# Performance work log

Measured on AMD Instinct MI355X. Metric: run time of the kernel, lower is better.

## Reference

```python
import jax, jax.numpy as jnp
import numpy as np

B, C, T, I, R = 32, 4, 512, 64, 1024
LEAK = 0.5          # reak_rate
DENSITY = 0.1       # reservoir_density
SPECTRAL_RADIUS = 0.95
W_SCALE = 1.0       # reservoir_weights_scale
IN_SCALE = 0.1      # input_weights_scale


def setup_inputs() -> dict:
    rng = np.random.default_rng(0)
    # reservoir weights: uniform, sparsified by density mask, rescaled so the
    # largest singular value equals the target spectral radius (as in __init__)
    W = rng.uniform(-W_SCALE, W_SCALE, (R, R)).astype(np.float32)
    mask = (rng.uniform(0.0, 1.0, (R, R)) < DENSITY).astype(np.float32)
    W = W * mask
    s_max = np.linalg.svd(W, compute_uv=False).max()
    W = W * (SPECTRAL_RADIUS / s_max)
    # input weights: [R, I*C]
    Wi = rng.uniform(-IN_SCALE, IN_SCALE, (R, I * C)).astype(np.float32)

    key = jax.random.key(0)
    x = jax.random.normal(key, (B, C, T, I), dtype=jnp.float32)
    return {
        "x": x,
        "input_weights": jnp.asarray(Wi),
        "reservoir_weights": jnp.asarray(W),
    }


def reference(x, input_weights, reservoir_weights):
    # x: [B, C, T, I]
    B_, C_, T_, I_ = x.shape
    R_ = reservoir_weights.shape[0]
    # precompute the input projection for all steps: u_t = flatten(x[:,:,t,:]) @ Wi.T
    xt = jnp.transpose(x, (2, 0, 1, 3)).reshape(T_, B_, C_ * I_)  # [T, B, C*I]
    U = xt @ input_weights.T                                       # [T, B, R]

    h0 = jnp.zeros((B_, C_, R_), dtype=x.dtype)  # per-channel reservoir state

    def step(h, u):
        # leaky-integrated reservoir update; input broadcasts over channels
        h_new = LEAK * jnp.tanh(u[:, None, :] + h @ reservoir_weights) + (1.0 - LEAK) * h
        return h_new, h_new

    _, hs = jax.lax.scan(step, h0, U)            # hs: [T, B, C, R]
    return jnp.transpose(hs, (1, 2, 0, 3))       # [B, C, T, R]
```

## Files before the change

### kernel.cpp

```cpp
#include <hip/hip_runtime.h>
#include <hip/hip_bf16.h>
#include <cstdint>
#include <cstddef>


typedef unsigned short u16;
typedef unsigned int   u32;
typedef unsigned long long u64;
typedef __bf16 bf16x8 __attribute__((ext_vector_type(8)));
typedef u64    u64x2  __attribute__((ext_vector_type(2)));
typedef float  f32x4  __attribute__((ext_vector_type(4)));
typedef float  f32x2  __attribute__((ext_vector_type(2)));

#define T_STEPS 512
#define NWG     256
#define TPB     256

#define OFF_WHI 0
#define OFF_U   (2*1024*1024)
#define OFF_HB  (OFF_U + (size_t)512*32*1024*4)
#define HB_BYTES ((size_t)128*2048)
#define OFF_BAR (OFF_HB + 2*HB_BYTES)

__device__ __forceinline__ u16 f2bf(float f) {
  u32 u = __builtin_bit_cast(u32, f);
  u += 0x7fffu + ((u >> 16) & 1u);
  return (u16)(u >> 16);
}
__device__ __forceinline__ float bf2f(u16 h) {
  u32 u = ((u32)h) << 16;
  return __builtin_bit_cast(float, u);
}
__device__ __forceinline__ void pinv(bf16x8& v) { asm volatile("" : "+v"(v)); }

__device__ __forceinline__ u32 AADD(u32* p, u32 v) {
  return __hip_atomic_fetch_add(p, v, __ATOMIC_RELAXED, __HIP_MEMORY_SCOPE_AGENT);
}
__device__ __forceinline__ u32 ALD(const u32* p) {
  return __hip_atomic_load(p, __ATOMIC_RELAXED, __HIP_MEMORY_SCOPE_AGENT);
}
__device__ __forceinline__ u64 ALD64(const u64* p) {
  return __hip_atomic_load(p, __ATOMIC_RELAXED, __HIP_MEMORY_SCOPE_AGENT);
}
__device__ __forceinline__ void AST(u32* p, u32 v) {
  __hip_atomic_store(p, v, __ATOMIC_RELAXED, __HIP_MEMORY_SCOPE_AGENT);
}

__global__ void prep_w(const float* __restrict__ W, u16* __restrict__ whi) {
  int n = blockIdx.y;
  int k = blockIdx.x * 256 + threadIdx.x;
  whi[n * 1024 + k] = f2bf(W[k * 1024 + n]);
}

__global__ void __launch_bounds__(256) prep_u2(const float* __restrict__ x,
                                               const float* __restrict__ Wi,
                                               float* __restrict__ U) {
  __shared__ __align__(16) u16 Ah[128 * 128];
  __shared__ __align__(16) u16 Al[128 * 128];
  const int tid = threadIdx.x;
  const int m0 = blockIdx.x << 7;
  const int n0 = blockIdx.y << 7;
  const int wv = tid >> 6, lane = tid & 63;
  const int fc = lane & 15, kb = lane >> 4;

  f32x4 acc[8][2];
#pragma unroll
  for (int mt = 0; mt < 8; ++mt) {
    acc[mt][0] = (f32x4){0.f, 0.f, 0.f, 0.f};
    acc[mt][1] = (f32x4){0.f, 0.f, 0.f, 0.f};
  }

  for (int hf = 0; hf < 2; ++hf) {
    __syncthreads();
#pragma unroll
    for (int s = 0; s < 16; ++s) {
      int f = (s << 8) + tid;
      int row = f >> 5, v = f & 31;
      int cl = v >> 4, i4 = (v & 15) << 2;
      int b = row & 31, t = (m0 + row) >> 5;
      float4 xv = *(const float4*)(x +
          ((size_t)((b << 2) | ((hf << 1) | cl)) * 512 + t) * 64 + i4);
      int byte = (row << 8) + (((cl << 7) + (i4 << 1)) ^ ((row & 7) << 4));
      u16* ph = (u16*)((char*)Ah + byte);
      u16* pl = (u16*)((char*)Al + byte);
      float vv[4] = {xv.x, xv.y, xv.z, xv.w};
#pragma unroll
      for (int e = 0; e < 4; ++e) {
        u16 hh = f2bf(vv[e]);
        ph[e] = hh;
        pl[e] = f2bf(vv[e] - bf2f(hh));
      }
    }
    bf16x8 Bh[2][4], Bl[2][4];
#pragma unroll
    for (int nt = 0; nt < 2; ++nt) {
      const float* wrow = Wi + (size_t)(n0 + (wv << 5) + (nt << 4) + fc) * 256;
#pragma unroll
      for (int kt = 0; kt < 4; ++kt) {
        int k = (hf << 7) + (kt << 5) + (kb << 3);
        float tmp[8];
        *(float4*)&tmp[0] = *(const float4*)(wrow + k);
        *(float4*)&tmp[4] = *(const float4*)(wrow + k + 4);
#pragma unroll
        for (int e = 0; e < 8; ++e) {
          u16 hh = f2bf(tmp[e]);
          Bh[nt][kt][e] = __builtin_bit_cast(__bf16, hh);
          Bl[nt][kt][e] = __builtin_bit_cast(__bf16, f2bf(tmp[e] - bf2f(hh)));
        }
      }
    }
    __syncthreads();
#pragma unroll
    for (int kt = 0; kt < 4; ++kt) {
      int kbyte = (kt << 6) + (kb << 4);
#pragma unroll
      for (int mt = 0; mt < 8; ++mt) {
        int row = (mt << 4) + fc;
        int byte = (row << 8) + (kbyte ^ ((row & 7) << 4));
        bf16x8 ah = *(const bf16x8*)((char*)Ah + byte);
        bf16x8 al = *(const bf16x8*)((char*)Al + byte);
#pragma unroll
        for (int nt = 0; nt < 2; ++nt) {
          acc[mt][nt] = __builtin_amdgcn_mfma_f32_16x16x32_bf16(ah, Bh[nt][kt], acc[mt][nt], 0, 0, 0);
          acc[mt][nt] = __builtin_amdgcn_mfma_f32_16x16x32_bf16(al, Bh[nt][kt], acc[mt][nt], 0, 0, 0);
          acc[mt][nt] = __builtin_amdgcn_mfma_f32_16x16x32_bf16(ah, Bl[nt][kt], acc[mt][nt], 0, 0, 0);
        }
      }
    }
  }
#pragma unroll
  for (int mt = 0; mt < 8; ++mt) {
    int mbase = m0 + (mt << 4) + (kb << 2);
    int n = n0 + (wv << 5) + fc;
#pragma unroll
    for (int nt = 0; nt < 2; ++nt)
#pragma unroll
      for (int r = 0; r < 4; ++r)
        U[(size_t)(mbase + r) * 1024 + n + (nt << 4)] = acc[mt][nt][r];
  }
}

__global__ void __launch_bounds__(TPB, 1) esn_scan(
    const u16* __restrict__ Whi, const float* __restrict__ U,
    u16* __restrict__ Hb, float* __restrict__ out, u32* __restrict__ bar) {
  __shared__ __align__(16) float red[8 * 64 * 4];
  __shared__ int sh_q, sh_j, sh_loc;

  const int tid = threadIdx.x;
  const int wv = tid >> 6, lane = tid & 63;
  const int mcol = lane & 15, kb = lane >> 4;

  if (tid == 0) {
    int xcd;
    asm volatile("s_getreg_b32 %0, hwreg(HW_REG_XCC_ID)" : "=s"(xcd));
    xcd &= 7;
    AADD(bar + xcd * 64, 1u);
    AADD(bar + 512, 1u);
    while (ALD(bar + 512) < (u32)NWG) __builtin_amdgcn_s_sleep(2);
    bool uni = true;
    for (int k = 0; k < 8; ++k) uni &= (ALD(bar + k * 64) == 32u);
    if (uni) {
      sh_q = xcd;
      sh_j = (int)AADD(bar + (9 + xcd) * 64, 1u);
      sh_loc = 1;
    } else {
      sh_q = blockIdx.x & 7;
      sh_j = blockIdx.x >> 3;
      sh_loc = 0;
    }
  }
  __syncthreads();
  const int q = sh_q, j = sh_j;
  const bool xlocal = (sh_loc != 0);
  const int r0 = q << 4, c0 = j << 5;

  bf16x8 bh[2][8];
#pragma unroll
  for (int nt = 0; nt < 2; ++nt) {
    const char* wb = (const char*)Whi + (size_t)(c0 + nt * 16 + mcol) * 2048
                     + wv * 512 + kb * 16;
#pragma unroll
    for (int kt = 0; kt < 8; ++kt)
      bh[nt][kt] = *(const bf16x8*)(wb + kt * 64);
  }
#pragma unroll
  for (int nt = 0; nt < 2; ++nt)
#pragma unroll
    for (int kt = 0; kt < 8; ++kt) pinv(bh[nt][kt]);

  const int row_l = tid >> 4;
  const int col0  = (tid & 15) * 2;
  const int grow  = r0 + row_l;
  const int ont   = col0 >> 4, oci = col0 & 15;
  const int okb   = row_l >> 2, orr = row_l & 3;
  u32* flags = bar + 2048 + q * 64;

  float hreg[2] = {0.f, 0.f};
  float po0 = 0.f, po1 = 0.f;
  f32x2 uf = *(const f32x2*)(U + (size_t)(grow >> 2) * 1024 + c0 + col0);

  for (int t = 0; t < T_STEPS; ++t) {
    const char* hsrc = (const char*)Hb + (size_t)(t & 1) * HB_BYTES
                       + (size_t)(r0 + mcol) * 2048 + wv * 512 + kb * 16;
    bf16x8 av[8];
    if (xlocal) {
#pragma unroll
      for (int kt = 0; kt < 8; ++kt)
        av[kt] = *(const bf16x8*)(hsrc + kt * 64);
    } else {
#pragma unroll
      for (int kt = 0; kt < 8; ++kt) {
        u64x2 p;
        p.x = ALD64((const u64*)(hsrc + kt * 64));
        p.y = ALD64((const u64*)(hsrc + kt * 64 + 8));
        av[kt] = __builtin_bit_cast(bf16x8, p);
      }
    }
    f32x2 ufn = uf;
    if (t < T_STEPS - 1)
      ufn = *(const f32x2*)(U + ((size_t)(t + 1) * 32 + (grow >> 2)) * 1024 + c0 + col0);
    __builtin_amdgcn_sched_barrier(0);
    if (t > 0) {
      f32x2 o2; o2.x = po0; o2.y = po1;
      __builtin_nontemporal_store(o2,
          (f32x2*)(out + ((size_t)grow * 512 + (t - 1)) * 1024 + c0 + col0));
    }
    __builtin_amdgcn_sched_barrier(0);

    f32x4 acc0 = {0.f, 0.f, 0.f, 0.f};
    f32x4 acc1 = {0.f, 0.f, 0.f, 0.f};
#pragma unroll
    for (int kt = 0; kt < 8; ++kt) {
      acc0 = __builtin_amdgcn_mfma_f32_16x16x32_bf16(av[kt], bh[0][kt], acc0, 0, 0, 0);
      acc1 = __builtin_amdgcn_mfma_f32_16x16x32_bf16(av[kt], bh[1][kt], acc1, 0, 0, 0);
    }

    *(f32x4*)&red[((wv * 2 + 0) * 64 + lane) * 4] = acc0;
    *(f32x4*)&red[((wv * 2 + 1) * 64 + lane) * 4] = acc1;
    __syncthreads();

    float z0 = 0.f, z1 = 0.f;
#pragma unroll
    for (int w = 0; w < 4; ++w) {
      z0 += red[((w * 2 + ont) * 64 + okb * 16 + oci + 0) * 4 + orr];
      z1 += red[((w * 2 + ont) * 64 + okb * 16 + oci + 1) * 4 + orr];
    }
    float hn0 = 0.5f * tanhf(z0 + uf.x) + 0.5f * hreg[0];
    float hn1 = 0.5f * tanhf(z1 + uf.y) + 0.5f * hreg[1];
    hreg[0] = hn0; hreg[1] = hn1;
    po0 = hn0; po1 = hn1;

    {
      u32 pk = (u32)f2bf(hn0) | ((u32)f2bf(hn1) << 16);
      u32* hdst = (u32*)((char*)Hb + (size_t)((t + 1) & 1) * HB_BYTES
                         + (size_t)grow * 2048 + (c0 + col0) * 2);
      if (xlocal) {
        *hdst = pk;
      } else {
        (void)__hip_atomic_exchange(hdst, pk, __ATOMIC_RELAXED,
                                    __HIP_MEMORY_SCOPE_AGENT);
      }
    }
    asm volatile("s_waitcnt vmcnt(0)" ::: "memory");
    __syncthreads();

    if (t < T_STEPS - 1) {
      if (tid == 0) {
        if (xlocal) *(volatile u32*)(flags + j) = (u32)(t + 1);
        else        AST(flags + j, (u32)(t + 1));
      }
      if (wv == 0) {
        u32 tgt = (u32)(t + 1);
        if (xlocal) {
          const u32* fp = flags + (lane & 31);
          while (true) {
            u32 v = ALD(fp);
            if (__all((int)(v >= tgt))) break;
          }
          asm volatile("buffer_inv\n\ts_waitcnt vmcnt(0)" ::: "memory");
        } else {
          while (true) {
            u32 v = ALD(flags + (lane & 31));
            if (__all((int)(v >= tgt))) break;
            __builtin_amdgcn_s_sleep(1);
          }
        }
      }
      __syncthreads();
    }
    uf = ufn;
  }
  {
    f32x2 o2; o2.x = po0; o2.y = po1;
    __builtin_nontemporal_store(o2,
        (f32x2*)(out + ((size_t)grow * 512 + (T_STEPS - 1)) * 1024 + c0 + col0));
  }
}

extern "C" void kernel_launch(void* const* d_in, const int* in_sizes, int n_in,
                              void* d_out, int out_size, void* d_ws, size_t ws_size,
                              hipStream_t stream) {
  (void)in_sizes; (void)n_in; (void)out_size; (void)ws_size;
  const float* x  = (const float*)d_in[0];
  const float* Wi = (const float*)d_in[1];
  const float* W  = (const float*)d_in[2];
  float* out = (float*)d_out;

  char* ws  = (char*)d_ws;
  u16*  whi = (u16*)(ws + OFF_WHI);
  float* U  = (float*)(ws + OFF_U);
  u16*  hb  = (u16*)(ws + OFF_HB);
  u32*  bar = (u32*)(ws + OFF_BAR);

  (void)hipMemsetAsync(ws + OFF_HB, 0, 2 * HB_BYTES + 16384, stream);

  hipLaunchKernelGGL(prep_w, dim3(4, 1024), dim3(256), 0, stream, W, whi);
  hipLaunchKernelGGL(prep_u2, dim3(128, 8), dim3(256), 0, stream, x, Wi, U);
  hipLaunchKernelGGL(esn_scan, dim3(NWG), dim3(TPB), 0, stream,
                     whi, U, hb, out, bar);
}
```

Baseline: 1.435 ms.

## Replace per-block barrier with per-wave flags and double-buffered reduction scratch

Each wave now publishes its own progress flag and polls the flags of the matching waves in the other workgroups. This removes the two block-wide __syncthreads around the cross-workgroup flag exchange. The LDS reduction buffer is double-buffered by timestep parity so that dropping the trailing barrier does not cause a write-after-read hazard. H loads always use the atomic 64-bit path and the buffer_inv on the local path is removed. This risks visibility or ordering issues and adds more polling traffic, since four times as many flags are now written and polled.

```diff
diff --git a/kernel.cpp b/kernel.cpp
--- a/kernel.cpp
+++ b/kernel.cpp
@@ -143,7 +143,7 @@
 __global__ void __launch_bounds__(TPB, 1) esn_scan(
     const u16* __restrict__ Whi, const float* __restrict__ U,
     u16* __restrict__ Hb, float* __restrict__ out, u32* __restrict__ bar) {
-  __shared__ __align__(16) float red[8 * 64 * 4];
+  __shared__ __align__(16) float red[2][8 * 64 * 4];
   __shared__ int sh_q, sh_j, sh_loc;
 
   const int tid = threadIdx.x;
@@ -193,7 +193,9 @@
   const int grow  = r0 + row_l;
   const int ont   = col0 >> 4, oci = col0 & 15;
   const int okb   = row_l >> 2, orr = row_l & 3;
-  u32* flags = bar + 2048 + q * 64;
+  u32* gflags = bar + 2048 + q * 128;
+  u32* myslot = gflags + (j << 2) + wv;
+  const u32* pollp = gflags + (wv << 5) + (lane & 31);
 
   float hreg[2] = {0.f, 0.f};
   float po0 = 0.f, po1 = 0.f;
@@ -203,18 +205,12 @@
     const char* hsrc = (const char*)Hb + (size_t)(t & 1) * HB_BYTES
                        + (size_t)(r0 + mcol) * 2048 + wv * 512 + kb * 16;
     bf16x8 av[8];
-    if (xlocal) {
-#pragma unroll
-      for (int kt = 0; kt < 8; ++kt)
-        av[kt] = *(const bf16x8*)(hsrc + kt * 64);
-    } else {
-#pragma unroll
-      for (int kt = 0; kt < 8; ++kt) {
-        u64x2 p;
-        p.x = ALD64((const u64*)(hsrc + kt * 64));
-        p.y = ALD64((const u64*)(hsrc + kt * 64 + 8));
-        av[kt] = __builtin_bit_cast(bf16x8, p);
-      }
+#pragma unroll
+    for (int kt = 0; kt < 8; ++kt) {
+      u64x2 p;
+      p.x = ALD64((const u64*)(hsrc + kt * 64));
+      p.y = ALD64((const u64*)(hsrc + kt * 64 + 8));
+      av[kt] = __builtin_bit_cast(bf16x8, p);
     }
     f32x2 ufn = uf;
     if (t < T_STEPS - 1)
@@ -235,15 +231,16 @@
       acc1 = __builtin_amdgcn_mfma_f32_16x16x32_bf16(av[kt], bh[1][kt], acc1, 0, 0, 0);
     }
 
-    *(f32x4*)&red[((wv * 2 + 0) * 64 + lane) * 4] = acc0;
-    *(f32x4*)&red[((wv * 2 + 1) * 64 + lane) * 4] = acc1;
+    float* rb = red[t & 1];
+    *(f32x4*)&rb[((wv * 2 + 0) * 64 + lane) * 4] = acc0;
+    *(f32x4*)&rb[((wv * 2 + 1) * 64 + lane) * 4] = acc1;
     __syncthreads();
 
     float z0 = 0.f, z1 = 0.f;
 #pragma unroll
     for (int w = 0; w < 4; ++w) {
-      z0 += red[((w * 2 + ont) * 64 + okb * 16 + oci + 0) * 4 + orr];
-      z1 += red[((w * 2 + ont) * 64 + okb * 16 + oci + 1) * 4 + orr];
+      z0 += rb[((w * 2 + ont) * 64 + okb * 16 + oci + 0) * 4 + orr];
+      z1 += rb[((w * 2 + ont) * 64 + okb * 16 + oci + 1) * 4 + orr];
     }
     float hn0 = 0.5f * tanhf(z0 + uf.x) + 0.5f * hreg[0];
     float hn1 = 0.5f * tanhf(z1 + uf.y) + 0.5f * hreg[1];
@@ -262,31 +259,25 @@
       }
     }
     asm volatile("s_waitcnt vmcnt(0)" ::: "memory");
-    __syncthreads();
 
     if (t < T_STEPS - 1) {
-      if (tid == 0) {
-        if (xlocal) *(volatile u32*)(flags + j) = (u32)(t + 1);
-        else        AST(flags + j, (u32)(t + 1));
-      }
-      if (wv == 0) {
-        u32 tgt = (u32)(t + 1);
-        if (xlocal) {
-          const u32* fp = flags + (lane & 31);
-          while (true) {
-            u32 v = ALD(fp);
-            if (__all((int)(v >= tgt))) break;
-          }
-          asm volatile("buffer_inv\n\ts_waitcnt vmcnt(0)" ::: "memory");
-        } else {
-          while (true) {
-            u32 v = ALD(flags + (lane & 31));
-            if (__all((int)(v >= tgt))) break;
-            __builtin_amdgcn_s_sleep(1);
-          }
+      if (lane == 0) {
+        if (xlocal) *(volatile u32*)myslot = (u32)(t + 1);
+        else        AST(myslot, (u32)(t + 1));
+      }
+      u32 tgt = (u32)(t + 1);
+      if (xlocal) {
+        while (true) {
+          u32 v = ALD(pollp);
+          if (__all((int)(v >= tgt))) break;
         }
-      }
-      __syncthreads();
+      } else {
+        while (true) {
+          u32 v = ALD(pollp);
+          if (__all((int)(v >= tgt))) break;
+          __builtin_amdgcn_s_sleep(1);
+        }
+      }
     }
     uf = ufn;
   }
```

Result: slower. 1.943 ms (+35.4%).

## Replace per-block barrier with per-wave flag slots in inter-block step sync

Applied to the files above, without the earlier changes.

Each wave now publishes its own completion flag (four slots per block), so the __syncthreads before signalling is dropped and waves signal as soon as their stores drain. The poller in wave 0 reads 128 slots instead of 32. The non-local path also loads h with plain vector loads instead of paired atomic 64-bit loads. This aims to cut per-step barrier latency in the 512-step recurrence, but it risks stale reads on the cross-XCD path, where plain loads may hit cached data without the invalidate that the local path issues.

```diff
diff --git a/kernel.cpp b/kernel.cpp
--- a/kernel.cpp
+++ b/kernel.cpp
@@ -193,7 +193,8 @@
   const int grow  = r0 + row_l;
   const int ont   = col0 >> 4, oci = col0 & 15;
   const int okb   = row_l >> 2, orr = row_l & 3;
-  u32* flags = bar + 2048 + q * 64;
+  u32* gflags = bar + 2048 + q * 128;
+  u32* myslot = gflags + (j << 2) + wv;
 
   float hreg[2] = {0.f, 0.f};
   float po0 = 0.f, po1 = 0.f;
@@ -203,19 +204,9 @@
     const char* hsrc = (const char*)Hb + (size_t)(t & 1) * HB_BYTES
                        + (size_t)(r0 + mcol) * 2048 + wv * 512 + kb * 16;
     bf16x8 av[8];
-    if (xlocal) {
-#pragma unroll
-      for (int kt = 0; kt < 8; ++kt)
-        av[kt] = *(const bf16x8*)(hsrc + kt * 64);
-    } else {
-#pragma unroll
-      for (int kt = 0; kt < 8; ++kt) {
-        u64x2 p;
-        p.x = ALD64((const u64*)(hsrc + kt * 64));
-        p.y = ALD64((const u64*)(hsrc + kt * 64 + 8));
-        av[kt] = __builtin_bit_cast(bf16x8, p);
-      }
-    }
+#pragma unroll
+    for (int kt = 0; kt < 8; ++kt)
+      av[kt] = *(const bf16x8*)(hsrc + kt * 64);
     f32x2 ufn = uf;
     if (t < T_STEPS - 1)
       ufn = *(const f32x2*)(U + ((size_t)(t + 1) * 32 + (grow >> 2)) * 1024 + c0 + col0);
@@ -262,26 +253,28 @@
       }
     }
     asm volatile("s_waitcnt vmcnt(0)" ::: "memory");
-    __syncthreads();
 
     if (t < T_STEPS - 1) {
-      if (tid == 0) {
-        if (xlocal) *(volatile u32*)(flags + j) = (u32)(t + 1);
-        else        AST(flags + j, (u32)(t + 1));
+      if (lane == 0) {
+        if (xlocal) *(volatile u32*)myslot = (u32)(t + 1);
+        else        AST(myslot, (u32)(t + 1));
       }
       if (wv == 0) {
         u32 tgt = (u32)(t + 1);
+        const u32* p0 = gflags + lane;
+        const u32* p1 = gflags + 64 + lane;
         if (xlocal) {
-          const u32* fp = flags + (lane & 31);
           while (true) {
-            u32 v = ALD(fp);
-            if (__all((int)(v >= tgt))) break;
+            u32 a = ALD(p0);
+            u32 b = ALD(p1);
+            if (__all((int)((a >= tgt) & (b >= tgt)))) break;
           }
           asm volatile("buffer_inv\n\ts_waitcnt vmcnt(0)" ::: "memory");
         } else {
           while (true) {
-            u32 v = ALD(flags + (lane & 31));
-            if (__all((int)(v >= tgt))) break;
+            u32 a = ALD(p0);
+            u32 b = ALD(p1);
+            if (__all((int)((a >= tgt) & (b >= tgt)))) break;
             __builtin_amdgcn_s_sleep(1);
           }
         }
```

New measurement: 1.499 ms. 4.4% more time.
